# Optimization experiments

Measured on AMD Instinct MI355X. Metric: run time of the kernel, lower is better.

Reference implementation:

```python
import jax, jax.numpy as jnp
import numpy as np
from jax import lax

WD, H, B, SQ, SS, CL = 300, 100, 128, 48, 48, 16
VOCAB, CVOCAB, CD, K = 91557, 53, 16, 3


def setup_inputs() -> dict:
    key = jax.random.key(0)
    ks = jax.random.split(key, 40)
    p = lambda i, shape: jax.random.normal(ks[i], shape, jnp.float32) * 0.02
    inp = {
        'q_words': jax.random.randint(ks[0], (B, SQ), 0, VOCAB),
        'q_chars': jax.random.randint(ks[1], (B, SQ, CL), 0, CVOCAB),
        's_words': jax.random.randint(ks[2], (B, SS), 0, VOCAB),
        's_chars': jax.random.randint(ks[3], (B, SS, CL), 0, CVOCAB),
        'word_emb': p(4, (VOCAB, WD)),
        'char_emb': p(5, (CVOCAB, CD)),
        'conv_w': p(6, (CD, 1, K)),
        'conv_b': p(7, (CD,)),
    }
    din = WD + CD
    for k in range(5):
        d = din + 2 * H * k  # dense connectivity: input grows by 2H per layer
        inp[f'wih{k+1}'] = p(8 + 4 * k, (4 * H, d))
        inp[f'whh{k+1}'] = p(9 + 4 * k, (4 * H, H))
        inp[f'bih{k+1}'] = p(10 + 4 * k, (4 * H,))
        inp[f'bhh{k+1}'] = p(11 + 4 * k, (4 * H,))
    inp['fcl_w'] = p(30, (800, 5 * H))
    inp['fcl_b'] = p(31, (800,))
    inp['last_w'] = p(32, (2, 800))
    inp['last_b'] = p(33, (2,))
    return inp


def _lstm_scan(x, wih, whh, bih, bhh):
    # x: [S, B, D] -> hidden states [S, B, H]; zero initial state (PyTorch LSTMCell default)
    h0 = jnp.zeros((x.shape[1], H), x.dtype)
    def step(carry, xt):
        h, c = carry
        g = xt @ wih.T + bih + h @ whh.T + bhh
        i, f, gg, o = jnp.split(g, 4, axis=-1)
        c = jax.nn.sigmoid(f) * c + jax.nn.sigmoid(i) * jnp.tanh(gg)
        h = jax.nn.sigmoid(o) * jnp.tanh(c)
        return (h, c), h
    _, hs = lax.scan(step, (h0, h0), x)
    return hs


def _embed(words, chars, word_emb, char_emb, conv_w, conv_b):
    w_e = word_emb[words]  # [B, S, WD]
    Bn, S, Cl = chars.shape
    ce = char_emb[chars].reshape(Bn * S, 1, Cl * CD)  # flatten chars per token
    raw = lax.conv_general_dilated(ce, conv_w, (1,), 'VALID',
                                   dimension_numbers=('NCH', 'OIH', 'NCH'))
    raw = (raw + conv_b[None, :, None]).reshape(Bn, S, CD, -1)
    pooled = jnp.max(jax.nn.relu(raw), axis=-1)        # [B, S, CD]
    pooled0 = jnp.max(raw[0], axis=-1)                 # original quirk: batch row 0 has no relu
    char_e = pooled.at[0].set(pooled0)
    return jnp.concatenate([w_e, char_e], axis=2).transpose(1, 0, 2)  # [S, B, WD+CD]


def _forward(q_words, q_chars, s_words, s_chars, word_emb, char_emb, conv_w, conv_b,
             cells, fcl_w, fcl_b, last_w, last_b):
    px = _embed(q_words, q_chars, word_emb, char_emb, conv_w, conv_b)
    hx = _embed(s_words, s_chars, word_emb, char_emb, conv_w, conv_b)
    hps = hhs = None
    for (wih, whh, bih, bhh) in cells:
        p_h = _lstm_scan(px, wih, whh, bih, bhh)  # [Sp, B, H]
        h_h = _lstm_scan(hx, wih, whh, bih, bhh)  # [Sh, B, H]
        hps = p_h.transpose(1, 0, 2)              # [B, Sp, H]
        hhs = h_h.transpose(1, 0, 2)              # [B, Sh, H]
        attn = jnp.einsum('bph,bqh->bpq', hps, hhs)
        a_p = jnp.einsum('bpq,bqh->bph', jax.nn.softmax(attn, axis=2), hhs)
        a_h = jnp.einsum('bqp,bph->bqh', jax.nn.softmax(attn.transpose(0, 2, 1), axis=2), hps)
        px = jnp.concatenate([px, a_p.transpose(1, 0, 2), p_h], axis=2)
        hx = jnp.concatenate([hx, a_h.transpose(1, 0, 2), h_h], axis=2)
    hq = jnp.max(hps, axis=1)  # max-pool over time
    hs = jnp.max(hhs, axis=1)
    feats = jnp.concatenate([hq, hs, hs - hq, hq * hs, jnp.abs(hq - hs)], axis=1)
    out = jax.nn.relu(feats @ fcl_w.T + fcl_b) @ last_w.T + last_b
    return jax.nn.sigmoid(out)


def reference(q_words, q_chars, s_words, s_chars, word_emb, char_emb, conv_w, conv_b,
              wih1, whh1, bih1, bhh1, wih2, whh2, bih2, bhh2, wih3, whh3, bih3, bhh3,
              wih4, whh4, bih4, bhh4, wih5, whh5, bih5, bhh5,
              fcl_w, fcl_b, last_w, last_b):
    cells = [(wih1, whh1, bih1, bhh1), (wih2, whh2, bih2, bhh2), (wih3, whh3, bih3, bhh3),
             (wih4, whh4, bih4, bhh4), (wih5, whh5, bih5, bhh5)]
    return _forward(q_words, q_chars, s_words, s_chars, word_emb, char_emb, conv_w, conv_b,
                    cells, fcl_w, fcl_b, last_w, last_b)
```

## Files before the change

kernel.cpp:

```cpp
#include <hip/hip_runtime.h>

typedef unsigned short u16;
typedef unsigned int   u32;

#define B_   128
#define S_   48
#define H_   100
#define G_   400
#define PXP  1120

__device__ __forceinline__ float b2f(u16 u) {
    union { u32 i; float f; } v; v.i = ((u32)u) << 16; return v.f;
}
__device__ __forceinline__ u16 f2b(float f) {
    union { float f; u32 i; } v; v.f = f;
    u32 r = v.i + 0x7FFF + ((v.i >> 16) & 1);
    return (u16)(r >> 16);
}

__device__ __forceinline__ float fsig(float x) { return 1.f / (1.f + __expf(-x)); }
__device__ __forceinline__ float ftanh(float x) {
    const float t = __expf(-2.f * fabsf(x));
    const float r = (1.f - t) / (1.f + t);
    return copysignf(r, x);
}

__device__ __forceinline__ float rl(float v0, float v1, int u) {
    return __int_as_float(
        u < 64 ? __builtin_amdgcn_readlane(__float_as_int(v0), u)
               : __builtin_amdgcn_readlane(__float_as_int(v1), u - 64));
}

__device__ __forceinline__ float ldw(const void* p, long i, int bf) {
    return bf ? b2f(((const u16*)p)[i]) : ((const float*)p)[i];
}

__global__ __launch_bounds__(256) void detect_kernel(const void* wemb, int* flag)
{
    const int t = threadIdx.x;
    __shared__ int s;
    if (t == 0) s = 0;
    __syncthreads();
    int bad = 0;
    const u16* p = (const u16*)wemb;
    for (int i = t; i < 4096; i += 256) {
        float v = b2f(p[i]);
        if (!(fabsf(v) < 1e4f)) bad = 1;
    }
    if (bad) atomicOr(&s, 1);
    __syncthreads();
    if (t == 0) *flag = s ? 0 : 1;
}

__global__ __launch_bounds__(64) void embed_kernel(
    const int* __restrict__ qw, const int* __restrict__ qc,
    const int* __restrict__ sw, const int* __restrict__ sc,
    const void* __restrict__ wemb, const void* __restrict__ cemb,
    const void* __restrict__ cw, const void* __restrict__ cb,
    u16* __restrict__ px, u16* __restrict__ hx, const int* __restrict__ flagp)
{
    const int bf = *flagp;
    const int b = blockIdx.x, s = blockIdx.y, seq = blockIdx.z;
    const int* words = seq ? sw : qw;
    const int* chars = seq ? sc : qc;
    u16* dst = seq ? hx : px;
    const int t = threadIdx.x;

    u16* row = dst + (long)(s * B_ + b) * PXP;
    const int w = words[b * S_ + s];
    if (bf) {
        const u32* src = (const u32*)((const u16*)wemb + (long)w * 300);
        u32* d32 = (u32*)row;
        for (int d = t; d < 150; d += 64) d32[d] = src[d];
    } else {
        const float* src = (const float*)wemb + (long)w * 300;
        for (int d = t; d < 300; d += 64) row[d] = f2b(src[d]);
    }

    __shared__ float ce[256];
    const int* ch = chars + (b * S_ + s) * 16;
    for (int j = t; j < 256; j += 64) {
        int ci = ch[j >> 4];
        ce[j] = ldw(cemb, ci * 16 + (j & 15), bf);
    }
    __syncthreads();

    float cwr[3][16], cbr[16];
#pragma unroll
    for (int oc = 0; oc < 16; ++oc) {
        cbr[oc] = ldw(cb, oc, bf);
#pragma unroll
        for (int kk = 0; kk < 3; ++kk) cwr[kk][oc] = ldw(cw, oc * 3 + kk, bf);
    }

    float vmax[16];
#pragma unroll
    for (int oc = 0; oc < 16; ++oc) vmax[oc] = -1e30f;

    for (int p = t; p < 254; p += 64) {
        float c0 = ce[p], c1 = ce[p + 1], c2 = ce[p + 2];
#pragma unroll
        for (int oc = 0; oc < 16; ++oc) {
            float v = fmaf(c0, cwr[0][oc], fmaf(c1, cwr[1][oc], fmaf(c2, cwr[2][oc], cbr[oc])));
            vmax[oc] = fmaxf(vmax[oc], v);
        }
    }
#pragma unroll
    for (int m = 32; m; m >>= 1) {
#pragma unroll
        for (int oc = 0; oc < 16; ++oc)
            vmax[oc] = fmaxf(vmax[oc], __shfl_xor(vmax[oc], m));
    }
    if (t == 0) {
#pragma unroll
        for (int oc = 0; oc < 16; ++oc) {
            float v = vmax[oc];
            if (b != 0) v = fmaxf(v, 0.f);
            row[300 + oc] = f2b(v);
        }
    }
}

#if defined(__gfx950__)

typedef __attribute__((ext_vector_type(4))) float f32x4;
typedef __attribute__((ext_vector_type(8))) __bf16 bf16x8;
#define LDPB 72
#define BK   64

__device__ __forceinline__ void gload_lds16(const void* g, void* l) {
    __builtin_amdgcn_global_load_lds(
        (const __attribute__((address_space(1))) u32*)g,
        (__attribute__((address_space(3))) u32*)l, 16, 0, 0);
}

__global__ __launch_bounds__(256) void gemm_wih(
    const u16* __restrict__ px, const u16* __restrict__ hx,
    float* __restrict__ Xg_p, float* __restrict__ Xg_h,
    const void* __restrict__ wih, const void* __restrict__ bih,
    const void* __restrict__ bhh, int K, const int* __restrict__ flagp)
{
    const int bf = *flagp;
    const u16* A = blockIdx.z ? hx : px;
    float* C = blockIdx.z ? Xg_h : Xg_p;
    const int m0 = blockIdx.x * 128, n0 = blockIdx.y * 64;

    __shared__ __align__(16) u16 As[128 * 64];
    __shared__ __align__(16) u16 Bs[64 * LDPB];

    const int tid  = threadIdx.x;
    const int lane = tid & 63;
    const int w    = tid >> 6;
    const int fr   = lane & 15;
    const int fq   = lane >> 4;

    const int rb = tid >> 2;
    const int kb = (tid & 3) * 16;
    const int nB = n0 + rb;
    const int bok = nB < G_;

    const int arow = lane >> 3;
    const int achk = (lane & 7) ^ arow;
    const u16* aLane = A + (long)(m0 + w * 32 + arow) * PXP + achk * 8;

    const u16* wp = (const u16*)wih;
    const u16* bSrc = wp + (long)nB * K + kb;

    f32x4 acc[2][4] = {};

    const int nfull = K / BK;

    for (int t = 0; t < nfull; ++t) {
        const int k0 = t * BK;
#pragma unroll
        for (int c = 0; c < 4; ++c)
            gload_lds16(aLane + (long)c * 8 * PXP + k0,
                        &As[(w * 32 + c * 8) * 64]);
        {
            u16* bs = &Bs[rb * LDPB + kb];
            if (bok) {
                const u16* bp = bSrc + k0;
#pragma unroll
                for (int i = 0; i < 4; ++i)
                    *(uint2*)(bs + i * 4) = *(const uint2*)(bp + i * 4);
            } else {
#pragma unroll
                for (int i = 0; i < 16; ++i) bs[i] = 0;
            }
        }
        __syncthreads();

#pragma unroll
        for (int ks = 0; ks < BK; ks += 32) {
            const int sw = (((ks >> 3) + fq) ^ (fr & 7)) * 8;
            bf16x8 a0 = *(const bf16x8*)&As[(w * 32 + fr) * 64 + sw];
            bf16x8 a1 = *(const bf16x8*)&As[(w * 32 + 16 + fr) * 64 + sw];
#pragma unroll
            for (int j = 0; j < 4; ++j) {
                bf16x8 bj = *(const bf16x8*)&Bs[(j * 16 + fr) * LDPB + ks + fq * 8];
                acc[0][j] = __builtin_amdgcn_mfma_f32_16x16x32_bf16(a0, bj, acc[0][j], 0, 0, 0);
                acc[1][j] = __builtin_amdgcn_mfma_f32_16x16x32_bf16(a1, bj, acc[1][j], 0, 0, 0);
            }
        }
        __syncthreads();
    }

    const int k0 = nfull * BK;
    if (k0 < K) {
        {
            const int ra = tid >> 1;
            const int ka = (tid & 1) * 32;
            const u16* ar = A + (long)(m0 + ra) * PXP;
            u16* bs = &Bs[rb * LDPB + kb];
            const u16* br = wp + (long)nB * K;
#pragma unroll
            for (int i = 0; i < 32; ++i) {
                const int o = ka + i;
                const int k = k0 + o;
                As[ra * 64 + (((o >> 3) ^ (ra & 7)) * 8) + (o & 7)] =
                    (k < K) ? ar[k] : (u16)0;
            }
#pragma unroll
            for (int i = 0; i < 16; ++i) {
                const int k = k0 + kb + i;
                bs[i] = (bok && k < K) ? br[k] : (u16)0;
            }
        }
        __syncthreads();
#pragma unroll
        for (int ks = 0; ks < BK; ks += 32) {
            const int sw = (((ks >> 3) + fq) ^ (fr & 7)) * 8;
            bf16x8 a0 = *(const bf16x8*)&As[(w * 32 + fr) * 64 + sw];
            bf16x8 a1 = *(const bf16x8*)&As[(w * 32 + 16 + fr) * 64 + sw];
#pragma unroll
            for (int j = 0; j < 4; ++j) {
                bf16x8 bj = *(const bf16x8*)&Bs[(j * 16 + fr) * LDPB + ks + fq * 8];
                acc[0][j] = __builtin_amdgcn_mfma_f32_16x16x32_bf16(a0, bj, acc[0][j], 0, 0, 0);
                acc[1][j] = __builtin_amdgcn_mfma_f32_16x16x32_bf16(a1, bj, acc[1][j], 0, 0, 0);
            }
        }
    }

#pragma unroll
    for (int j = 0; j < 4; ++j) {
        const int col = n0 + j * 16 + fr;
        if (col < G_) {
            const float bias = ldw(bih, col, bf) + ldw(bhh, col, bf);
#pragma unroll
            for (int m = 0; m < 2; ++m)
#pragma unroll
                for (int i = 0; i < 4; ++i) {
                    const int row = m0 + w * 32 + m * 16 + fq * 4 + i;
                    C[(long)row * G_ + col] = acc[m][j][i] + bias;
                }
        }
    }
}
#undef LDPB
#undef BK

#else

__global__ __launch_bounds__(256) void gemm_wih(
    const u16* __restrict__ px, const u16* __restrict__ hx,
    float* __restrict__ Xg_p, float* __restrict__ Xg_h,
    const void* __restrict__ wih, const void* __restrict__ bih,
    const void* __restrict__ bhh, int K, const int* __restrict__ flagp)
{
    const int bf = *flagp;
    const u16* A = blockIdx.z ? hx : px;
    float* C = blockIdx.z ? Xg_h : Xg_p;

    __shared__ float As[16][64];
    __shared__ float Bs[16][64];

    const int tid = threadIdx.x;
    const int tx = tid & 15, ty = tid >> 4;
    const int m0 = blockIdx.x * 64, n0 = blockIdx.y * 64;
    const int lr = tid >> 2, lk = (tid & 3) * 4;

    float acc[4][4] = {};

    for (int k0 = 0; k0 < K; k0 += 16) {
        const u16* Ap = A + (long)(m0 + lr) * PXP + k0 + lk;
#pragma unroll
        for (int u = 0; u < 4; ++u)
            As[lk + u][lr] = (k0 + lk + u < K) ? b2f(Ap[u]) : 0.f;
        {
            const int n = n0 + lr;
#pragma unroll
            for (int u = 0; u < 4; ++u) {
                const int kk = k0 + lk + u;
                Bs[lk + u][lr] = (n < G_ && kk < K) ? ldw(wih, (long)n * K + kk, bf) : 0.f;
            }
        }
        __syncthreads();
#pragma unroll
        for (int k = 0; k < 16; ++k) {
            float a[4], bq[4];
#pragma unroll
            for (int i = 0; i < 4; ++i) a[i] = As[k][ty * 4 + i];
#pragma unroll
            for (int j = 0; j < 4; ++j) bq[j] = Bs[k][tx * 4 + j];
#pragma unroll
            for (int i = 0; i < 4; ++i)
#pragma unroll
                for (int j = 0; j < 4; ++j)
                    acc[i][j] = fmaf(a[i], bq[j], acc[i][j]);
        }
        __syncthreads();
    }

#pragma unroll
    for (int j = 0; j < 4; ++j) {
        const int col = n0 + tx * 4 + j;
        if (col < G_) {
            const float bias = ldw(bih, col, bf) + ldw(bhh, col, bf);
#pragma unroll
            for (int i = 0; i < 4; ++i)
                C[(long)(m0 + ty * 4 + i) * G_ + col] = acc[i][j] + bias;
        }
    }
}

#endif

__global__ __launch_bounds__(448, 2)
void lstm_scan(
    const float* __restrict__ Xg_p, const float* __restrict__ Xg_h,
    const void* __restrict__ whh,
    float* __restrict__ p_h, float* __restrict__ h_h,
    u16* __restrict__ px, u16* __restrict__ hx, int cat_off,
    const int* __restrict__ flagp)
{
    const int bf = *flagp;
    const int b = blockIdx.x, seq = blockIdx.y;
    const float* Xg = seq ? Xg_h : Xg_p;
    float* hout = seq ? h_h : p_h;
    u16* xcat = seq ? hx : px;
    const int g = threadIdx.x;
    const int l = g & 63;

    __shared__ float h_lds[128];
    __shared__ float g_lds[400];
    __shared__ float h_hist[S_ * 104];

    u32 wpk[50];
    float xg = 0.f;
    if (g < G_) {
        if (bf) {
            const u32* w2 = (const u32*)whh;
#pragma unroll
            for (int j = 0; j < 50; ++j) wpk[j] = w2[g * 50 + j];
        } else {
            const float* wf = (const float*)whh;
#pragma unroll
            for (int j = 0; j < 50; ++j) {
                u32 lo = f2b(wf[(long)g * 100 + 2 * j]);
                u32 hi = f2b(wf[(long)g * 100 + 2 * j + 1]);
                wpk[j] = lo | (hi << 16);
            }
        }
#pragma unroll
        for (int j = 0; j < 50; ++j) asm volatile("" : "+v"(wpk[j]));
        xg = Xg[(long)b * G_ + g];
    }
    if (g < 128) h_lds[g] = 0.f;
    float c_reg = 0.f;
    __syncthreads();

    for (int s = 0; s < S_; ++s) {
        const float hv0 = h_lds[l];
        const float hv1 = h_lds[l + 64];
        if (g < G_) {
            float a0 = xg, a1 = 0.f, a2 = 0.f, a3 = 0.f;
#pragma unroll
            for (int u = 0; u < 100; u += 4) {
                const u32 p0 = wpk[u >> 1], p1 = wpk[(u >> 1) + 1];
                const float w0 = __int_as_float(p0 << 16);
                const float w1 = __int_as_float(p0 & 0xFFFF0000u);
                const float w2 = __int_as_float(p1 << 16);
                const float w3 = __int_as_float(p1 & 0xFFFF0000u);
                a0 = fmaf(rl(hv0, hv1, u),     w0, a0);
                a1 = fmaf(rl(hv0, hv1, u + 1), w1, a1);
                a2 = fmaf(rl(hv0, hv1, u + 2), w2, a2);
                a3 = fmaf(rl(hv0, hv1, u + 3), w3, a3);
            }
            g_lds[g] = (a0 + a1) + (a2 + a3);
            if (s + 1 < S_) xg = Xg[(long)((s + 1) * B_ + b) * G_ + g];
        }
        __syncthreads();
        if (g < H_) {
            const float iv = fsig(g_lds[g]);
            const float fv = fsig(g_lds[100 + g]);
            const float gv = ftanh(g_lds[200 + g]);
            const float ov = fsig(g_lds[300 + g]);
            c_reg = fv * c_reg + iv * gv;
            const float hv = ov * ftanh(c_reg);
            h_lds[g] = hv;
            h_hist[s * 104 + g] = hv;
        }
        __syncthreads();
    }

    for (int i = g; i < S_ * H_; i += 448) {
        const int s = i / H_, d = i - s * H_;
        const float hv = h_hist[s * 104 + d];
        hout[(long)(s * B_ + b) * H_ + d] = hv;
        if (cat_off >= 0) xcat[(long)(s * B_ + b) * PXP + cat_off + d] = f2b(hv);
    }
}

__global__ __launch_bounds__(256) void attn_kernel(
    const float* __restrict__ p_h, const float* __restrict__ h_h,
    u16* __restrict__ px, u16* __restrict__ hx, int off)
{
    const int b = blockIdx.x, dir = blockIdx.y, t = threadIdx.x;
    __shared__ __align__(16) float P[4800], Q[4800];
    __shared__ float A[2304], Sx[2304];

    {
        float4* P4 = (float4*)P;
        float4* Q4 = (float4*)Q;
        for (int i = t; i < 1200; i += 256) {
            const int s = i / 25, d4 = i % 25;
            P4[i] = *(const float4*)(p_h + (long)(s * B_ + b) * H_ + d4 * 4);
            Q4[i] = *(const float4*)(h_h + (long)(s * B_ + b) * H_ + d4 * 4);
        }
    }
    __syncthreads();

    for (int e = t; e < 2304; e += 256) {
        const int p = e / 48, q = e % 48;
        const float4* Pr = (const float4*)&P[p * 100];
        const float4* Qr = (const float4*)&Q[q * 100];
        float a0 = 0.f, a1 = 0.f;
#pragma unroll
        for (int j = 0; j < 25; ++j) {
            const float4 u = Pr[j], v = Qr[j];
            a0 = fmaf(u.x, v.x, a0); a1 = fmaf(u.y, v.y, a1);
            a0 = fmaf(u.z, v.z, a0); a1 = fmaf(u.w, v.w, a1);
        }
        A[e] = a0 + a1;
    }
    __syncthreads();

    if (t < 48) {
        if (dir == 0) {
            float m = -1e30f;
            for (int q = 0; q < 48; ++q) m = fmaxf(m, A[t * 48 + q]);
            float sum = 0.f;
            for (int q = 0; q < 48; ++q) sum += __expf(A[t * 48 + q] - m);
            const float inv = 1.f / sum;
            for (int q = 0; q < 48; ++q) Sx[t * 48 + q] = __expf(A[t * 48 + q] - m) * inv;
        } else {
            float m = -1e30f;
            for (int p = 0; p < 48; ++p) m = fmaxf(m, A[p * 48 + t]);
            float sum = 0.f;
            for (int p = 0; p < 48; ++p) sum += __expf(A[p * 48 + t] - m);
            const float inv = 1.f / sum;
            for (int p = 0; p < 48; ++p) Sx[p * 48 + t] = __expf(A[p * 48 + t] - m) * inv;
        }
    }
    __syncthreads();

    if (dir == 0) {
        for (int e = t; e < 4800; e += 256) {
            const int p = e / 100, d = e % 100;
            float acc = 0.f;
            for (int q = 0; q < 48; ++q) acc = fmaf(Sx[p * 48 + q], Q[q * 100 + d], acc);
            px[(long)(p * B_ + b) * PXP + off + d] = f2b(acc);
        }
    } else {
        for (int e = t; e < 4800; e += 256) {
            const int q = e / 100, d = e % 100;
            float acc = 0.f;
            for (int p = 0; p < 48; ++p) acc = fmaf(Sx[p * 48 + q], P[p * 100 + d], acc);
            hx[(long)(q * B_ + b) * PXP + off + d] = f2b(acc);
        }
    }
}

__global__ __launch_bounds__(256) void pool_feats(
    const float* __restrict__ p_h, const float* __restrict__ h_h,
    float* __restrict__ feats)
{
    const int t = blockIdx.x * 256 + threadIdx.x;
    if (t >= B_ * H_) return;
    const int b = t / H_, u = t % H_;
    float hq = -1e30f, hs = -1e30f;
    for (int s = 0; s < S_; ++s) {
        hq = fmaxf(hq, p_h[(long)(s * B_ + b) * H_ + u]);
        hs = fmaxf(hs, h_h[(long)(s * B_ + b) * H_ + u]);
    }
    float* f = feats + b * 500;
    f[u]       = hq;
    f[100 + u] = hs;
    f[200 + u] = hs - hq;
    f[300 + u] = hq * hs;
    f[400 + u] = fabsf(hq - hs);
}

__global__ __launch_bounds__(256) void fcl_kernel(
    const float* __restrict__ feats, const void* __restrict__ fw,
    const void* __restrict__ fb, float* __restrict__ z, const int* __restrict__ flagp)
{
    const int bf = *flagp;
    const int t = blockIdx.x * 256 + threadIdx.x;
    const int o = t >> 7, b = t & 127;
    float acc = ldw(fb, o, bf);
    const float* f = feats + b * 500;
    for (int d = 0; d < 500; ++d) acc = fmaf(f[d], ldw(fw, (long)o * 500 + d, bf), acc);
    z[b * 800 + o] = fmaxf(acc, 0.f);
}

__global__ __launch_bounds__(256) void last_kernel(
    const float* __restrict__ z, const void* __restrict__ lw,
    const void* __restrict__ lb, void* __restrict__ out, const int* __restrict__ flagp)
{
    const int bf = *flagp;
    const int t = threadIdx.x;
    const int b = t >> 1, c = t & 1;
    float acc = ldw(lb, c, bf);
    const float* zr = z + b * 800;
    for (int o = 0; o < 800; ++o) acc = fmaf(zr[o], ldw(lw, (long)c * 800 + o, bf), acc);
    const float v = 1.f / (1.f + expf(-acc));
    if (bf) ((u16*)out)[t] = f2b(v);
    else    ((float*)out)[t] = v;
}

extern "C" void kernel_launch(void* const* d_in, const int* in_sizes, int n_in,
                              void* d_out, int out_size, void* d_ws, size_t ws_size,
                              hipStream_t stream)
{
    (void)in_sizes; (void)n_in; (void)out_size; (void)ws_size;

    const int* qw = (const int*)d_in[0];
    const int* qc = (const int*)d_in[1];
    const int* sw = (const int*)d_in[2];
    const int* sc = (const int*)d_in[3];
    const void* wemb = d_in[4];
    const void* cemb = d_in[5];
    const void* cw   = d_in[6];
    const void* cb   = d_in[7];
    const void* fclw = d_in[28];
    const void* fclb = d_in[29];
    const void* lw   = d_in[30];
    const void* lb   = d_in[31];

    float* ws = (float*)d_ws;
    int*  flag = (int*)ws;
    u16* px   = (u16*)(ws + 16);
    u16* hx   = px + (long)S_ * B_ * PXP;
    float* Xg_p = (float*)(hx + (long)S_ * B_ * PXP);
    float* Xg_h = Xg_p + (long)S_ * B_ * G_;
    float* p_h  = Xg_h + (long)S_ * B_ * G_;
    float* h_h  = p_h + (long)S_ * B_ * H_;
    float* feats = h_h + (long)S_ * B_ * H_;
    float* z    = feats + B_ * 500;

    detect_kernel<<<dim3(1), 256, 0, stream>>>(wemb, flag);

    embed_kernel<<<dim3(B_, S_, 2), 64, 0, stream>>>(qw, qc, sw, sc, wemb, cemb, cw, cb, px, hx, flag);

    for (int k = 0; k < 5; ++k) {
        const void* wih = d_in[8 + 4 * k];
        const void* whh = d_in[9 + 4 * k];
        const void* bih = d_in[10 + 4 * k];
        const void* bhh = d_in[11 + 4 * k];
        const int K = 316 + 200 * k;

        gemm_wih<<<dim3(48, 7, 2), 256, 0, stream>>>(px, hx, Xg_p, Xg_h, wih, bih, bhh, K, flag);

        const int cat = (k < 4) ? (K + 100) : -1;
        lstm_scan<<<dim3(B_, 2), 448, 0, stream>>>(Xg_p, Xg_h, whh, p_h, h_h, px, hx, cat, flag);

        if (k < 4)
            attn_kernel<<<dim3(B_, 2), 256, 0, stream>>>(p_h, h_h, px, hx, K);
    }

    pool_feats<<<dim3(50), 256, 0, stream>>>(p_h, h_h, feats);
    fcl_kernel<<<dim3(400), 256, 0, stream>>>(feats, fclw, fclb, z, flag);
    last_kernel<<<dim3(1), 256, 0, stream>>>(z, lw, lb, d_out, flag);
}
```

Baseline: 879.6 us.

## Double-buffer LDS tiles in input-projection GEMM to overlap loads with MFMA

Splits the A and B shared-memory tiles into two ping-pong buffers so the next K-tile is fetched (direct global-to-LDS for A, registers then LDS for B) while MFMAs run on the current one. The two barriers per iteration become one explicit waitcnt plus barrier. In exchange LDS use doubles, which may lower occupancy, and the B write still waits on its global load before compute, so the overlap is partial. This targets only the gemm_wih kernel, and the sequential LSTM recurrence probably accounts for much of the total time.

```diff
diff --git a/kernel.cpp b/kernel.cpp
--- a/kernel.cpp
+++ b/kernel.cpp
@@ -145,8 +145,10 @@
     float* C = blockIdx.z ? Xg_h : Xg_p;
     const int m0 = blockIdx.x * 128, n0 = blockIdx.y * 64;
 
-    __shared__ __align__(16) u16 As[128 * 64];
-    __shared__ __align__(16) u16 Bs[64 * LDPB];
+    __shared__ __align__(16) u16 As0[128 * 64];
+    __shared__ __align__(16) u16 As1[128 * 64];
+    __shared__ __align__(16) u16 Bs0[64 * LDPB];
+    __shared__ __align__(16) u16 Bs1[64 * LDPB];
 
     const int tid  = threadIdx.x;
     const int lane = tid & 63;
@@ -168,41 +170,77 @@
 
     f32x4 acc[2][4] = {};
 
-    const int nfull = K / BK;
-
-    for (int t = 0; t < nfull; ++t) {
-        const int k0 = t * BK;
+    auto loadB = [&](int k0, uint2* br4) {
+        if (bok) {
+            const u16* bp = bSrc + k0;
+#pragma unroll
+            for (int i = 0; i < 4; ++i) br4[i] = *(const uint2*)(bp + i * 4);
+        } else {
+#pragma unroll
+            for (int i = 0; i < 4; ++i) { br4[i].x = 0u; br4[i].y = 0u; }
+        }
+    };
+    auto stageA = [&](u16* dstAs, int k0) {
 #pragma unroll
         for (int c = 0; c < 4; ++c)
             gload_lds16(aLane + (long)c * 8 * PXP + k0,
-                        &As[(w * 32 + c * 8) * 64]);
-        {
-            u16* bs = &Bs[rb * LDPB + kb];
-            if (bok) {
-                const u16* bp = bSrc + k0;
-#pragma unroll
-                for (int i = 0; i < 4; ++i)
-                    *(uint2*)(bs + i * 4) = *(const uint2*)(bp + i * 4);
-            } else {
-#pragma unroll
-                for (int i = 0; i < 16; ++i) bs[i] = 0;
-            }
-        }
-        __syncthreads();
-
+                        &dstAs[(w * 32 + c * 8) * 64]);
+    };
+    auto writeB = [&](u16* dstBs, const uint2* br4) {
+        u16* bs = &dstBs[rb * LDPB + kb];
+#pragma unroll
+        for (int i = 0; i < 4; ++i) *(uint2*)(bs + i * 4) = br4[i];
+    };
+    auto compute = [&](const u16* As_, const u16* Bs_) {
 #pragma unroll
         for (int ks = 0; ks < BK; ks += 32) {
             const int sw = (((ks >> 3) + fq) ^ (fr & 7)) * 8;
-            bf16x8 a0 = *(const bf16x8*)&As[(w * 32 + fr) * 64 + sw];
-            bf16x8 a1 = *(const bf16x8*)&As[(w * 32 + 16 + fr) * 64 + sw];
+            bf16x8 a0 = *(const bf16x8*)&As_[(w * 32 + fr) * 64 + sw];
+            bf16x8 a1 = *(const bf16x8*)&As_[(w * 32 + 16 + fr) * 64 + sw];
 #pragma unroll
             for (int j = 0; j < 4; ++j) {
-                bf16x8 bj = *(const bf16x8*)&Bs[(j * 16 + fr) * LDPB + ks + fq * 8];
+                bf16x8 bj = *(const bf16x8*)&Bs_[(j * 16 + fr) * LDPB + ks + fq * 8];
                 acc[0][j] = __builtin_amdgcn_mfma_f32_16x16x32_bf16(a0, bj, acc[0][j], 0, 0, 0);
                 acc[1][j] = __builtin_amdgcn_mfma_f32_16x16x32_bf16(a1, bj, acc[1][j], 0, 0, 0);
             }
         }
-        __syncthreads();
+    };
+
+    const int nfull = K / BK;
+
+    {
+        uint2 br4[4];
+        loadB(0, br4);
+        stageA(As0, 0);
+        writeB(Bs0, br4);
+    }
+    asm volatile("s_waitcnt vmcnt(0) lgkmcnt(0)" ::: "memory");
+    __builtin_amdgcn_s_barrier();
+
+    int t = 0;
+    while (t < nfull) {
+        if (t + 1 < nfull) {
+            uint2 br4[4];
+            loadB((t + 1) * BK, br4);
+            stageA(As1, (t + 1) * BK);
+            writeB(Bs1, br4);
+        }
+        compute(As0, Bs0);
+        asm volatile("s_waitcnt vmcnt(0) lgkmcnt(0)" ::: "memory");
+        __builtin_amdgcn_s_barrier();
+        ++t;
+        if (t >= nfull) break;
+
+        if (t + 1 < nfull) {
+            uint2 br4[4];
+            loadB((t + 1) * BK, br4);
+            stageA(As0, (t + 1) * BK);
+            writeB(Bs0, br4);
+        }
+        compute(As1, Bs1);
+        asm volatile("s_waitcnt vmcnt(0) lgkmcnt(0)" ::: "memory");
+        __builtin_amdgcn_s_barrier();
+        ++t;
     }
 
     const int k0 = nfull * BK;
@@ -211,13 +249,13 @@
             const int ra = tid >> 1;
             const int ka = (tid & 1) * 32;
             const u16* ar = A + (long)(m0 + ra) * PXP;
-            u16* bs = &Bs[rb * LDPB + kb];
+            u16* bs = &Bs0[rb * LDPB + kb];
             const u16* br = wp + (long)nB * K;
 #pragma unroll
             for (int i = 0; i < 32; ++i) {
                 const int o = ka + i;
                 const int k = k0 + o;
-                As[ra * 64 + (((o >> 3) ^ (ra & 7)) * 8) + (o & 7)] =
+                As0[ra * 64 + (((o >> 3) ^ (ra & 7)) * 8) + (o & 7)] =
                     (k < K) ? ar[k] : (u16)0;
             }
 #pragma unroll
@@ -227,18 +265,7 @@
             }
         }
         __syncthreads();
-#pragma unroll
-        for (int ks = 0; ks < BK; ks += 32) {
-            const int sw = (((ks >> 3) + fq) ^ (fr & 7)) * 8;
-            bf16x8 a0 = *(const bf16x8*)&As[(w * 32 + fr) * 64 + sw];
-            bf16x8 a1 = *(const bf16x8*)&As[(w * 32 + 16 + fr) * 64 + sw];
-#pragma unroll
-            for (int j = 0; j < 4; ++j) {
-                bf16x8 bj = *(const bf16x8*)&Bs[(j * 16 + fr) * LDPB + ks + fq * 8];
-                acc[0][j] = __builtin_amdgcn_mfma_f32_16x16x32_bf16(a0, bj, acc[0][j], 0, 0, 0);
-                acc[1][j] = __builtin_amdgcn_mfma_f32_16x16x32_bf16(a1, bj, acc[1][j], 0, 0, 0);
-            }
-        }
+        compute(As0, Bs0);
     }
 
 #pragma unroll
```

Result: no change. 875.8 us (-0.4%).
